# Optimization experiments

Hardware: AMD Instinct MI355X
Metric: run time of the kernel (lower is better)

The kernel has to match this reference:

```python
import jax, jax.numpy as jnp
import numpy as np

B, N, C, H = 16, 1024, 768, 12
HD = C // H               # head_dim = 64
SCALE = HD ** -0.5
EPS = 1e-5


def ter_quant(w):
    """BitNet-b1.58 ternary weight quantization with straight-through estimator.
    Per-tensor scale = mean(|W|); weights rounded to {-1,0,1}*scale."""
    s = jnp.mean(jnp.abs(w))
    wq = jnp.round(jnp.clip(w / (s + EPS), -1.0, 1.0)) * s
    return w + jax.lax.stop_gradient(wq - w)


def setup_inputs() -> dict:
    key = jax.random.key(0)
    k1, k2, k3 = jax.random.split(key, 3)
    return {
        "x": jax.random.normal(k1, (B, N, C), dtype=jnp.float32),
        "w_qkv": jax.random.normal(k2, (3 * C, C), dtype=jnp.float32) * 0.02,
        "w_proj": jax.random.normal(k3, (C, C), dtype=jnp.float32) * 0.02,
        "b_proj": jnp.zeros((C,), dtype=jnp.float32),
    }


def reference(x, w_qkv, w_proj, b_proj):
    # ternary-quantized QKV projection: [B,N,C] @ [C,3C] -> [B,N,3C]
    qkv = jnp.einsum('bnc,dc->bnd', x, ter_quant(w_qkv))
    qkv = qkv.reshape(B, N, 3, H, HD).transpose(2, 0, 3, 1, 4)  # [3,B,H,N,HD]
    q, k, v = qkv[0], qkv[1], qkv[2]
    # manual softmax attention (dropout p=0 -> identity)
    attn = jax.nn.softmax(jnp.einsum('bhqd,bhkd->bhqk', q, k) * SCALE, axis=-1)
    out = jnp.einsum('bhqk,bhkd->bhqd', attn, v)          # [B,H,N,HD]
    out = out.transpose(0, 2, 1, 3).reshape(B, N, C)      # [B,N,C]
    # ternary-quantized output projection
    return jnp.einsum('bnc,dc->bnd', out, ter_quant(w_proj)) + b_proj
```

## Files before the change

kernel.cpp:

```cpp
#include <hip/hip_runtime.h>
#include <hip/hip_bf16.h>

#define DEVI __device__ __forceinline__

typedef __bf16 bf16_t;
typedef __bf16 bf16x8 __attribute__((ext_vector_type(8)));
typedef float  f32x4  __attribute__((ext_vector_type(4)));
typedef float  f32x16 __attribute__((ext_vector_type(16)));
typedef unsigned short u16x4 __attribute__((ext_vector_type(4)));
typedef unsigned int   u32x4 __attribute__((ext_vector_type(4)));

typedef __attribute__((address_space(1))) unsigned int gas_u32;
typedef __attribute__((address_space(3))) unsigned int las_u32;

#define LOG2E 1.4426950408889634f

DEVI void gload16(const void* g, void* l) {
  __builtin_amdgcn_global_load_lds((gas_u32*)g, (las_u32*)l, 16, 0, 0);
}

DEVI unsigned short bf16bits(float f) {
  bf16_t b = (bf16_t)f;
  return __builtin_bit_cast(unsigned short, b);
}

DEVI unsigned pk2(float a, float b) {
  return ((unsigned)bf16bits(b) << 16) | (unsigned)bf16bits(a);
}

__global__ __launch_bounds__(256) void k_abssum(const float* __restrict__ w, int n,
                                                double* __restrict__ partials) {
  __shared__ double sm[256];
  const int t = threadIdx.x;
  double acc = 0.0;
  for (int i = blockIdx.x * 256 + t; i < n; i += 256 * 256)
    acc += (double)fabsf(w[i]);
  sm[t] = acc;
  __syncthreads();
  #pragma unroll
  for (int s = 128; s > 0; s >>= 1) {
    if (t < s) sm[t] += sm[t + s];
    __syncthreads();
  }
  if (t == 0) partials[blockIdx.x] = sm[0];
}

__global__ __launch_bounds__(256) void k_reduce2(const double* __restrict__ partials,
                                                 double* __restrict__ outs) {
  __shared__ double sm[256];
  const int t = threadIdx.x;
  sm[t] = partials[blockIdx.x * 256 + t];
  __syncthreads();
  #pragma unroll
  for (int s = 128; s > 0; s >>= 1) {
    if (t < s) sm[t] += sm[t + s];
    __syncthreads();
  }
  if (t == 0) outs[blockIdx.x] = sm[0];
}

__global__ __launch_bounds__(256) void k_quant(const float* __restrict__ w,
                                               const double* __restrict__ sum, double invn,
                                               bf16_t* __restrict__ out) {
  const double s = (*sum) * invn + 1e-5;
  const int i = blockIdx.x * 256 + threadIdx.x;
  double tq = (double)w[i] / s;
  tq = fmin(fmax(tq, -1.0), 1.0);
  out[i] = (bf16_t)(float)rint(tq);
}

__global__ __launch_bounds__(256) void k_tobf16(const float* __restrict__ x,
                                                bf16_t* __restrict__ y) {
  const int i = blockIdx.x * 256 + threadIdx.x;
  const float4 v = ((const float4*)x)[i];
  u16x4 pk = { bf16bits(v.x), bf16bits(v.y), bf16bits(v.z), bf16bits(v.w) };
  ((u16x4*)y)[i] = pk;
}

template<int MODE>
__global__ __launch_bounds__(256) void k_gemm(
    const bf16_t* __restrict__ A, const bf16_t* __restrict__ Bw,
    const double* __restrict__ sumptr, double invn,
    bf16_t* __restrict__ Qb, bf16_t* __restrict__ Kb, bf16_t* __restrict__ VTb,
    const float* __restrict__ bias, float* __restrict__ Out,
    int nxblk)
{
  __shared__ bf16_t lds[2 * 128 * 64];
  bf16_t* lA = lds;
  bf16_t* lB = lds + 128 * 64;
  const int t = threadIdx.x, l = t & 63, w = t >> 6;

  const int nblk = nxblk * 128;
  const int flat = blockIdx.y * nxblk + blockIdx.x;
  const int per = nblk >> 3;
  const int swz = (flat % 8) * per + flat / 8;
  const int m0 = (swz / nxblk) * 128, n0 = (swz % nxblk) * 128;

  const int wr = w >> 1, wc = w & 1;
  const int srow = l >> 3, scol = (l & 7) * 8;
  const int lq = l & 15, lh = l >> 4;
  f32x4 acc[4][4] = {};
  for (int k0 = 0; k0 < 768; k0 += 64) {
    __syncthreads();
    #pragma unroll
    for (int i = 0; i < 4; ++i) {
      const int c = i * 4 + w;
      const int row = c * 8 + srow;
      const int gcol = scol ^ ((row & 7) * 8);
      gload16(A + (size_t)(m0 + row) * 768 + k0 + gcol, &lA[c * 512]);
    }
    #pragma unroll
    for (int i = 0; i < 4; ++i) {
      const int c = i * 4 + w;
      const int row = c * 8 + srow;
      const int gcol = scol ^ ((row & 7) * 8);
      gload16(Bw + (size_t)(n0 + row) * 768 + k0 + gcol, &lB[c * 512]);
    }
    __syncthreads();
    #pragma unroll
    for (int kb = 0; kb < 2; ++kb) {
      const int kByte = (kb * 32 + lh * 8) * 2;
      bf16x8 af[4], bf[4];
      #pragma unroll
      for (int i = 0; i < 4; ++i) {
        const int row = wr * 64 + i * 16 + lq;
        af[i] = *(const bf16x8*)((const char*)lA + row * 128 + (kByte ^ ((row & 7) << 4)));
      }
      #pragma unroll
      for (int j = 0; j < 4; ++j) {
        const int row = wc * 64 + j * 16 + lq;
        bf[j] = *(const bf16x8*)((const char*)lB + row * 128 + (kByte ^ ((row & 7) << 4)));
      }
      #pragma unroll
      for (int i = 0; i < 4; ++i)
        #pragma unroll
        for (int j = 0; j < 4; ++j)
          acc[i][j] = __builtin_amdgcn_mfma_f32_16x16x32_bf16(af[i], bf[j], acc[i][j], 0, 0, 0);
    }
  }
  __syncthreads();

  const float s = (float)((*sumptr) * invn);
  char* st = (char*)(lds + w * 4096);

  const int mrow0 = m0 + wr * 64;
  const int b = mrow0 >> 10, nbase = mrow0 & 1023;

  if (MODE == 0) {
    const int d0 = n0 + wc * 64;
    const int which = d0 / 768;
    const int hh = (d0 >> 6) % 12;
    if (which == 2) {
      #pragma unroll
      for (int j = 0; j < 4; ++j)
        #pragma unroll
        for (int i = 0; i < 4; ++i)
          #pragma unroll
          for (int r = 0; r < 4; ++r) {
            const int rowd = j * 16 + lq;
            const int coln = (i * 16 + lh * 4 + r) * 2;
            *(bf16_t*)(st + rowd * 128 + (coln ^ ((rowd & 7) << 4))) =
                (bf16_t)(acc[i][j][r] * s);
          }
    } else {
      const float sc = (which == 0) ? s * 0.125f * LOG2E : s;
      #pragma unroll
      for (int i = 0; i < 4; ++i)
        #pragma unroll
        for (int j = 0; j < 4; ++j)
          #pragma unroll
          for (int r = 0; r < 4; ++r) {
            const int row = i * 16 + lh * 4 + r;
            const int colb = (j * 16 + lq) * 2;
            *(bf16_t*)(st + row * 128 + (colb ^ ((row & 7) << 4))) =
                (bf16_t)(acc[i][j][r] * sc);
          }
    }
    __syncthreads();
    if (which == 2) {
      char* dstp = (char*)(VTb + ((size_t)(b * 12 + hh) * 64) * 1024 + nbase);
      #pragma unroll
      for (int it = 0; it < 8; ++it) {
        const int rowd = it * 8 + (l >> 3);
        const int coln = (l & 7) * 16;
        const u32x4 v = *(const u32x4*)(st + rowd * 128 + (coln ^ ((rowd & 7) << 4)));
        *(u32x4*)(dstp + rowd * 2048 + coln) = v;
      }
    } else {
      bf16_t* __restrict__ dst = (which == 0) ? Qb : Kb;
      char* dstp = (char*)(dst + ((size_t)(b * 12 + hh) * 1024 + nbase) * 64);
      #pragma unroll
      for (int it = 0; it < 8; ++it) {
        const int row = it * 8 + (l >> 3);
        const int colb = (l & 7) * 16;
        const u32x4 v = *(const u32x4*)(st + row * 128 + (colb ^ ((row & 7) << 4)));
        *(u32x4*)(dstp + row * 128 + colb) = v;
      }
    }
  } else {
    const int d0 = n0 + wc * 64;
    const float4 bv = *(const float4*)(bias + d0 + (l & 15) * 4);
    #pragma unroll
    for (int c = 0; c < 2; ++c) {
      #pragma unroll
      for (int i2 = 0; i2 < 2; ++i2) {
        const int i = c * 2 + i2;
        #pragma unroll
        for (int j = 0; j < 4; ++j)
          #pragma unroll
          for (int r = 0; r < 4; ++r) {
            const int row = i2 * 16 + lh * 4 + r;
            const int colb = (j * 16 + lq) * 4;
            *(float*)(st + row * 256 + (colb ^ ((row & 7) << 4))) = acc[i][j][r] * s;
          }
      }
      __syncthreads();
      #pragma unroll
      for (int it = 0; it < 8; ++it) {
        const int row = it * 4 + (l >> 4);
        const int colb = (l & 15) * 16;
        float4 v = *(const float4*)(st + row * 256 + (colb ^ ((row & 7) << 4)));
        v.x += bv.x; v.y += bv.y; v.z += bv.z; v.w += bv.w;
        *(float4*)((char*)(Out + (size_t)(mrow0 + c * 32 + row) * 768 + d0) + colb) = v;
      }
      __syncthreads();
    }
  }
}

__global__ __launch_bounds__(256, 3) void k_attn(
    const bf16_t* __restrict__ Qb, const bf16_t* __restrict__ Kb,
    const bf16_t* __restrict__ VTb, bf16_t* __restrict__ Ob)
{
  __shared__ bf16_t smem[2][2][4096];
  const int t = threadIdx.x, l = t & 63, w = t >> 6;
  const int bh = blockIdx.x, qb = blockIdx.y;
  const int lq = l & 31, hi = l >> 5;
  const int srow = l >> 3, scol = (l & 7) * 8;
  const int q0 = qb * 128 + w * 32;

  bf16x8 qf[4];
  #pragma unroll
  for (int ks = 0; ks < 4; ++ks)
    qf[ks] = *(const bf16x8*)(Qb + ((size_t)bh * 1024 + q0 + lq) * 64 + ks * 16 + hi * 8);

  f32x16 ot[2] = {};
  float mrun = -1e30f, lrun = 0.0f;

  auto stage = [&](int buf, int kt) {
    const int nn0 = kt * 64;
    #pragma unroll
    for (int i = 0; i < 2; ++i) {
      const int c = i * 4 + w;
      const int row = c * 8 + srow;
      const int gcol = scol ^ ((row & 7) * 8);
      gload16(Kb + ((size_t)bh * 1024 + nn0 + row) * 64 + gcol, &smem[buf][0][c * 512]);
      gload16(VTb + ((size_t)bh * 64 + row) * 1024 + nn0 + gcol, &smem[buf][1][c * 512]);
    }
  };

  stage(0, 0);
  __syncthreads();

  for (int kt = 0; kt < 16; ++kt) {
    const int cur = kt & 1;
    if (kt < 15) stage(cur ^ 1, kt + 1);
    const char* lK = (const char*)smem[cur][0];
    const char* lV = (const char*)smem[cur][1];

    f32x16 st[2] = {};
    __builtin_amdgcn_s_setprio(1);
    #pragma unroll
    for (int kt2 = 0; kt2 < 2; ++kt2) {
      #pragma unroll
      for (int ks = 0; ks < 4; ++ks) {
        const int row = kt2 * 32 + lq;
        const bf16x8 kf =
            *(const bf16x8*)(lK + row * 128 + ((ks * 32 + hi * 16) ^ ((row & 7) << 4)));
        st[kt2] = __builtin_amdgcn_mfma_f32_32x32x16_bf16(kf, qf[ks], st[kt2], 0, 0, 0);
      }
    }
    __builtin_amdgcn_s_setprio(0);

    float pmax = st[0][0];
    #pragma unroll
    for (int r = 1; r < 16; ++r) pmax = fmaxf(pmax, st[0][r]);
    #pragma unroll
    for (int r = 0; r < 16; ++r) pmax = fmaxf(pmax, st[1][r]);
    pmax = fmaxf(pmax, __shfl_xor(pmax, 32));

    if (__any(pmax > mrun + 8.0f)) {
      const float mn = fmaxf(mrun, pmax);
      const float corr = __builtin_amdgcn_exp2f(mrun - mn);
      lrun *= corr;
      #pragma unroll
      for (int dt = 0; dt < 2; ++dt)
        #pragma unroll
        for (int r = 0; r < 16; ++r) ot[dt][r] *= corr;
      mrun = mn;
    }

    float psum = 0.0f;
    __builtin_amdgcn_s_setprio(1);
    #pragma unroll
    for (int g = 0; g < 4; ++g) {
      const int tile = g >> 1, r0 = (g & 1) * 8;
      float p[8];
      #pragma unroll
      for (int e = 0; e < 8; ++e) {
        p[e] = __builtin_amdgcn_exp2f(st[tile][r0 + e] - mrun);
        psum += p[e];
      }
      const unsigned w0 = pk2(p[0], p[1]), w1 = pk2(p[2], p[3]);
      const unsigned w2 = pk2(p[4], p[5]), w3 = pk2(p[6], p[7]);
      const unsigned x0 = __shfl_xor(w0, 32), x1 = __shfl_xor(w1, 32);
      const unsigned x2 = __shfl_xor(w2, 32), x3 = __shfl_xor(w3, 32);
      const u32x4 fw = hi ? u32x4{x2, x3, w2, w3} : u32x4{w0, w1, x0, x1};
      const bf16x8 pf = __builtin_bit_cast(bf16x8, fw);
      #pragma unroll
      for (int dt = 0; dt < 2; ++dt) {
        const int row = dt * 32 + lq;
        const bf16x8 vf =
            *(const bf16x8*)(lV + row * 128 + ((g * 32 + hi * 16) ^ ((row & 7) << 4)));
        ot[dt] = __builtin_amdgcn_mfma_f32_32x32x16_bf16(vf, pf, ot[dt], 0, 0, 0);
      }
    }
    __builtin_amdgcn_s_setprio(0);
    psum += __shfl_xor(psum, 32);
    lrun += psum;

    __syncthreads();
  }

  __syncthreads();
  bf16_t* olds = (bf16_t*)smem + w * 2048;
  const float inv = 1.0f / lrun;
  #pragma unroll
  for (int dt = 0; dt < 2; ++dt)
    #pragma unroll
    for (int rg = 0; rg < 4; ++rg) {
      u16x4 pk;
      #pragma unroll
      for (int e = 0; e < 4; ++e) pk[e] = bf16bits(ot[dt][rg * 4 + e] * inv);
      const int d = rg * 8 + hi * 4 + dt * 32;
      *(u16x4*)((char*)olds + ((lq * 128 + d * 2) ^ ((lq & 7) << 4))) = pk;
    }
  __syncthreads();
  const int b = bh / 12, h = bh % 12;
  #pragma unroll
  for (int i = 0; i < 8; ++i) {
    const int q = i * 4 + (l >> 4);
    const u16x4 v =
        *(const u16x4*)((const char*)olds + ((q * 128 + (l & 15) * 8) ^ ((q & 7) << 4)));
    *(u16x4*)(Ob + ((size_t)(b * 1024 + q0 + q)) * 768 + h * 64 + (l & 15) * 4) = v;
  }
}

extern "C" void kernel_launch(void* const* d_in, const int* in_sizes, int n_in,
                              void* d_out, int out_size, void* d_ws, size_t ws_size,
                              hipStream_t stream) {
  const float* x      = (const float*)d_in[0];
  const float* w_qkv  = (const float*)d_in[1];
  const float* w_proj = (const float*)d_in[2];
  const float* b_proj = (const float*)d_in[3];
  float* out = (float*)d_out;

  char* ws = (char*)d_ws;
  double* part  = (double*)ws;
  double* scl   = (double*)(ws + 4096);
  bf16_t* xbf   = (bf16_t*)(ws + 4608);
  bf16_t* wqs   = (bf16_t*)(ws + 4608 + 25165824);
  bf16_t* wps   = (bf16_t*)(ws + 4608 + 25165824 + 3538944);
  bf16_t* qbuf  = (bf16_t*)(ws + 4608 + 25165824 + 3538944 + 1179648);
  bf16_t* kbuf  = qbuf + 12582912;
  bf16_t* vtbuf = kbuf + 12582912;
  bf16_t* aout  = xbf;

  k_abssum<<<256, 256, 0, stream>>>(w_qkv, 2304 * 768, part);
  k_abssum<<<256, 256, 0, stream>>>(w_proj, 768 * 768, part + 256);
  k_reduce2<<<2, 256, 0, stream>>>(part, scl);
  k_quant<<<6912, 256, 0, stream>>>(w_qkv, scl, 1.0 / 1769472.0, wqs);
  k_quant<<<2304, 256, 0, stream>>>(w_proj, scl + 1, 1.0 / 589824.0, wps);
  k_tobf16<<<12288, 256, 0, stream>>>(x, xbf);
  k_gemm<0><<<dim3(18, 128), 256, 0, stream>>>(xbf, wqs, scl, 1.0 / 1769472.0,
                                               qbuf, kbuf, vtbuf, nullptr, nullptr, 18);
  k_attn<<<dim3(192, 8), 256, 0, stream>>>(qbuf, kbuf, vtbuf, aout);
  k_gemm<1><<<dim3(6, 128), 256, 0, stream>>>(aout, wps, scl + 1, 1.0 / 589824.0,
                                              nullptr, nullptr, nullptr, b_proj, out, 6);
}
```

Before: 230.6 us.

## Triple-buffer GEMM LDS pipeline with 256x128 tiles and 512-thread blocks

Rewrites the bf16 GEMM main loop used for the QKV and output projections. The block tile grows to 256x128 with 8 waves. Global-to-LDS loads go into a three-slot ring buffer and are issued two k-tiles ahead, split across the two k-halves of each tile. Raw s_barrier and s_waitcnt vmcnt replace the paired __syncthreads, and s_setprio is raised around the MFMA bursts, all to hide global memory latency behind compute. The cost is 144 KB of LDS per block, which limits each CU to one block, and hand-placed waitcnt and barrier logic that is fragile.

After: 212.6 us. -7.8%, faster.

```diff
diff --git a/kernel.cpp b/kernel.cpp
--- a/kernel.cpp
+++ b/kernel.cpp
@@ -78,76 +78,112 @@
 }
 
 template<int MODE>
-__global__ __launch_bounds__(256) void k_gemm(
+__global__ __launch_bounds__(512, 2) void k_gemm(
     const bf16_t* __restrict__ A, const bf16_t* __restrict__ Bw,
     const double* __restrict__ sumptr, double invn,
     bf16_t* __restrict__ Qb, bf16_t* __restrict__ Kb, bf16_t* __restrict__ VTb,
     const float* __restrict__ bias, float* __restrict__ Out,
     int nxblk)
 {
-  __shared__ bf16_t lds[2 * 128 * 64];
-  bf16_t* lA = lds;
-  bf16_t* lB = lds + 128 * 64;
+  __shared__ __align__(16) char lds[147456];
   const int t = threadIdx.x, l = t & 63, w = t >> 6;
 
-  const int nblk = nxblk * 128;
+  const int nblk = nxblk * 64;
   const int flat = blockIdx.y * nxblk + blockIdx.x;
   const int per = nblk >> 3;
-  const int swz = (flat % 8) * per + flat / 8;
-  const int m0 = (swz / nxblk) * 128, n0 = (swz % nxblk) * 128;
-
-  const int wr = w >> 1, wc = w & 1;
+  const int swz = (flat & 7) * per + (flat >> 3);
+  const int m0 = (swz / nxblk) * 256, n0 = (swz % nxblk) * 128;
+
+  const int wm = w >> 1, wn = w & 1;
   const int srow = l >> 3, scol = (l & 7) * 8;
   const int lq = l & 15, lh = l >> 4;
+  const int gcol = scol ^ (srow * 8);
+
+  auto sA = [&](int slot, int kts, int ha, int c) {
+    const int row = ha * 128 + (c * 8 + w) * 8 + srow;
+    gload16(A + (size_t)(m0 + row) * 768 + kts * 64 + gcol,
+            lds + slot * 49152 + ha * 16384 + (c * 8 + w) * 1024);
+  };
+  auto sB = [&](int slot, int kts, int c) {
+    const int row = (c * 8 + w) * 8 + srow;
+    gload16(Bw + (size_t)(n0 + row) * 768 + kts * 64 + gcol,
+            lds + slot * 49152 + 32768 + (c * 8 + w) * 1024);
+  };
+
   f32x4 acc[4][4] = {};
-  for (int k0 = 0; k0 < 768; k0 += 64) {
-    __syncthreads();
-    #pragma unroll
-    for (int i = 0; i < 4; ++i) {
-      const int c = i * 4 + w;
-      const int row = c * 8 + srow;
-      const int gcol = scol ^ ((row & 7) * 8);
-      gload16(A + (size_t)(m0 + row) * 768 + k0 + gcol, &lA[c * 512]);
-    }
-    #pragma unroll
-    for (int i = 0; i < 4; ++i) {
-      const int c = i * 4 + w;
-      const int row = c * 8 + srow;
-      const int gcol = scol ^ ((row & 7) * 8);
-      gload16(Bw + (size_t)(n0 + row) * 768 + k0 + gcol, &lB[c * 512]);
-    }
-    __syncthreads();
-    #pragma unroll
-    for (int kb = 0; kb < 2; ++kb) {
-      const int kByte = (kb * 32 + lh * 8) * 2;
+
+  sA(0, 0, 0, 0); sA(0, 0, 0, 1); sA(0, 0, 1, 0); sA(0, 0, 1, 1);
+  sB(0, 0, 0);    sB(0, 0, 1);
+  sA(1, 1, 0, 0); sA(1, 1, 0, 1); sA(1, 1, 1, 0); sA(1, 1, 1, 1);
+  sB(1, 1, 0);    sB(1, 1, 1);
+  asm volatile("s_waitcnt vmcnt(6)" ::: "memory");
+  asm volatile("s_barrier" ::: "memory");
+
+  #pragma unroll
+  for (int kt = 0; kt < 12; ++kt) {
+    const char* cA = lds + (kt % 3) * 49152;
+    const char* cB = cA + 32768;
+    const int st3 = (kt + 2) % 3;
+    const bool stg = (kt < 10);
+
+    {
       bf16x8 af[4], bf[4];
       #pragma unroll
       for (int i = 0; i < 4; ++i) {
-        const int row = wr * 64 + i * 16 + lq;
-        af[i] = *(const bf16x8*)((const char*)lA + row * 128 + (kByte ^ ((row & 7) << 4)));
+        const int row = wm * 64 + i * 16 + lq;
+        af[i] = *(const bf16x8*)(cA + row * 128 + ((lh * 16) ^ ((row & 7) << 4)));
       }
       #pragma unroll
       for (int j = 0; j < 4; ++j) {
-        const int row = wc * 64 + j * 16 + lq;
-        bf[j] = *(const bf16x8*)((const char*)lB + row * 128 + (kByte ^ ((row & 7) << 4)));
-      }
+        const int row = wn * 64 + j * 16 + lq;
+        bf[j] = *(const bf16x8*)(cB + row * 128 + ((lh * 16) ^ ((row & 7) << 4)));
+      }
+      if (stg) { sA(st3, kt + 2, 0, 0); sA(st3, kt + 2, 0, 1); sB(st3, kt + 2, 0); }
+      asm volatile("s_barrier" ::: "memory");
+      __builtin_amdgcn_s_setprio(1);
       #pragma unroll
       for (int i = 0; i < 4; ++i)
         #pragma unroll
         for (int j = 0; j < 4; ++j)
           acc[i][j] = __builtin_amdgcn_mfma_f32_16x16x32_bf16(af[i], bf[j], acc[i][j], 0, 0, 0);
-    }
-  }
-  __syncthreads();
+      __builtin_amdgcn_s_setprio(0);
+      asm volatile("s_barrier" ::: "memory");
+    }
+    {
+      bf16x8 af[4], bf[4];
+      #pragma unroll
+      for (int i = 0; i < 4; ++i) {
+        const int row = wm * 64 + i * 16 + lq;
+        af[i] = *(const bf16x8*)(cA + row * 128 + ((64 + lh * 16) ^ ((row & 7) << 4)));
+      }
+      #pragma unroll
+      for (int j = 0; j < 4; ++j) {
+        const int row = wn * 64 + j * 16 + lq;
+        bf[j] = *(const bf16x8*)(cB + row * 128 + ((64 + lh * 16) ^ ((row & 7) << 4)));
+      }
+      if (stg) { sA(st3, kt + 2, 1, 0); sA(st3, kt + 2, 1, 1); sB(st3, kt + 2, 1); }
+      asm volatile("s_barrier" ::: "memory");
+      __builtin_amdgcn_s_setprio(1);
+      #pragma unroll
+      for (int i = 0; i < 4; ++i)
+        #pragma unroll
+        for (int j = 0; j < 4; ++j)
+          acc[i][j] = __builtin_amdgcn_mfma_f32_16x16x32_bf16(af[i], bf[j], acc[i][j], 0, 0, 0);
+      __builtin_amdgcn_s_setprio(0);
+      if (stg) asm volatile("s_waitcnt vmcnt(6)" ::: "memory");
+      else     asm volatile("s_waitcnt vmcnt(0)" ::: "memory");
+      asm volatile("s_barrier" ::: "memory");
+    }
+  }
 
   const float s = (float)((*sumptr) * invn);
-  char* st = (char*)(lds + w * 4096);
-
-  const int mrow0 = m0 + wr * 64;
+  char* st = lds + w * 8192;
+
+  const int mrow0 = m0 + wm * 64;
   const int b = mrow0 >> 10, nbase = mrow0 & 1023;
 
   if (MODE == 0) {
-    const int d0 = n0 + wc * 64;
+    const int d0 = n0 + wn * 64;
     const int which = d0 / 768;
     const int hh = (d0 >> 6) % 12;
     if (which == 2) {
@@ -198,7 +234,7 @@
       }
     }
   } else {
-    const int d0 = n0 + wc * 64;
+    const int d0 = n0 + wn * 64;
     const float4 bv = *(const float4*)(bias + d0 + (l & 15) * 4);
     #pragma unroll
     for (int c = 0; c < 2; ++c) {
@@ -382,9 +418,9 @@
   k_quant<<<6912, 256, 0, stream>>>(w_qkv, scl, 1.0 / 1769472.0, wqs);
   k_quant<<<2304, 256, 0, stream>>>(w_proj, scl + 1, 1.0 / 589824.0, wps);
   k_tobf16<<<12288, 256, 0, stream>>>(x, xbf);
-  k_gemm<0><<<dim3(18, 128), 256, 0, stream>>>(xbf, wqs, scl, 1.0 / 1769472.0,
-                                               qbuf, kbuf, vtbuf, nullptr, nullptr, 18);
+  k_gemm<0><<<dim3(18, 64), 512, 0, stream>>>(xbf, wqs, scl, 1.0 / 1769472.0,
+                                              qbuf, kbuf, vtbuf, nullptr, nullptr, 18);
   k_attn<<<dim3(192, 8), 256, 0, stream>>>(qbuf, kbuf, vtbuf, aout);
-  k_gemm<1><<<dim3(6, 128), 256, 0, stream>>>(aout, wps, scl + 1, 1.0 / 589824.0,
-                                              nullptr, nullptr, nullptr, b_proj, out, 6);
-}
+  k_gemm<1><<<dim3(6, 64), 512, 0, stream>>>(aout, wps, scl + 1, 1.0 / 589824.0,
+                                             nullptr, nullptr, nullptr, b_proj, out, 6);
+}
```
